# Kernel tuning notes

Hardware: AMD Instinct MI355X
Metric: run time of the kernel (lower is better)

The kernel has to match this reference:

```python
import jax, jax.numpy as jnp
import numpy as np

N_TOKENS = 65536
D_MODEL = 256
D_HID = 256
N_EXPERTS = 8


def setup_inputs() -> dict:
    key = jax.random.key(0)
    ks = jax.random.split(key, 6)
    x = jax.random.normal(ks[0], (N_TOKENS, D_MODEL), dtype=jnp.float32)
    # gate Linear weight [E, d] (torch Linear stores [out, in]); small init like nn.Linear default scale
    wg = jax.random.normal(ks[1], (N_EXPERTS, D_MODEL), dtype=jnp.float32) * 0.06
    W1 = jax.random.normal(ks[2], (N_EXPERTS, D_MODEL, D_HID), dtype=jnp.float32) * 0.06
    b1 = jnp.zeros((N_EXPERTS, D_HID), dtype=jnp.float32)
    W2 = jax.random.normal(ks[3], (N_EXPERTS, D_HID, D_MODEL), dtype=jnp.float32) * 0.06
    b2 = jnp.zeros((N_EXPERTS, D_MODEL), dtype=jnp.float32)
    return {"x": x, "wg": wg, "W1": W1, "b1": b1, "W2": W2, "b2": b2}


def reference(x, wg, W1, b1, W2, b2):
    # Gate: logits = x @ wg.T ; softmax over experts ; top-1 gate value + assignment
    gates = jax.nn.softmax(x @ wg.T, axis=1)                  # [N, E]
    gate_val = jnp.max(gates, axis=1)                          # [N] == topk(k=1) values
    assign = jnp.argmax(gates, axis=1)                         # [N] expert id per token

    out = jnp.zeros_like(x)
    # Fixed small loop over experts (structural, not data-dim); each iter is one dense GEMM pair.
    for e in range(N_EXPERTS):
        h = jax.nn.relu(x @ W1[e] + b1[e])                     # [N, D_HID]
        y_e = h @ W2[e] + b2[e]                                # [N, D_MODEL]
        sel = (assign == e)[:, None]
        out = jnp.where(sel, y_e * gate_val[:, None], out)
    return out
```

## Files before the change

kernel.cpp:

```cpp
#include <hip/hip_runtime.h>
#include <hip/hip_bf16.h>
#include <math.h>

#define NTOK 65536
#define DMODEL 256
#define NEXP 8
#define CAP 65536
#define MAXTILES 1040
#define CSTRIDE 64

typedef __bf16 bf16_t;
typedef __bf16 bf16x8 __attribute__((ext_vector_type(8)));
typedef float f32x4 __attribute__((ext_vector_type(4)));

__device__ inline void async16(const void* g, void* l) {
  __builtin_amdgcn_global_load_lds(
      (const __attribute__((address_space(1))) unsigned int*)g,
      (__attribute__((address_space(3))) unsigned int*)l, 16, 0, 0);
}

__global__ void prep_kernel(const float* __restrict__ wg, float* __restrict__ wgT,
                            int* __restrict__ counts) {
  int t = blockIdx.x * 256 + threadIdx.x;
  if (t < NEXP * DMODEL) wgT[t] = wg[(t & 7) * 256 + (t >> 3)];
  if (t < NEXP * CSTRIDE) counts[t] = 0;
}

__global__ __launch_bounds__(256) void castT_kernel(
    const float* __restrict__ W1, const float* __restrict__ W2,
    bf16_t* __restrict__ w1t, bf16_t* __restrict__ w2t) {
  __shared__ float tile[32][33];
  const int m = blockIdx.z;
  const float* src = (m < 8) ? (W1 + (size_t)m * 65536) : (W2 + (size_t)(m - 8) * 65536);
  bf16_t* dst = (m < 8) ? (w1t + (size_t)m * 65536) : (w2t + (size_t)(m - 8) * 65536);
  const int x0 = blockIdx.x * 32, y0 = blockIdx.y * 32;
  const int tx = threadIdx.x, ty = threadIdx.y;
#pragma unroll
  for (int i = 0; i < 4; ++i)
    tile[ty + i * 8][tx] = src[(size_t)(y0 + ty + i * 8) * 256 + x0 + tx];
  __syncthreads();
#pragma unroll
  for (int i = 0; i < 4; ++i)
    dst[(size_t)(x0 + ty + i * 8) * 256 + y0 + tx] = (bf16_t)tile[tx][ty + i * 8];
}

__global__ __launch_bounds__(256) void gate_kernel(
    const float* __restrict__ x, const float* __restrict__ wgT,
    bf16_t* __restrict__ xb, float* __restrict__ gateval,
    int* __restrict__ counts, int* __restrict__ idxbuf) {
  __shared__ __align__(16) float xs[64 * 256];
  __shared__ double part[3][64][9];
  const int th = threadIdx.x;
  const int lane = th & 63;
  const int wv = th >> 6;
  const int tokbase = blockIdx.x * 64;

#pragma unroll
  for (int i = 0; i < 16; ++i) {
    int p = i * 256 + th;
    int r = p >> 6;
    int c = (p & 63) ^ (r & 31);
    async16(x + (size_t)(tokbase + r) * 256 + c * 4,
            &xs[(i * 256 + wv * 64) * 4]);
  }
  __syncthreads();

#pragma unroll
  for (int i = 0; i < 8; ++i) {
    int p = i * 256 + th;
    int r = p >> 5, cb = p & 31;
    int mk = r & 31;
    f32x4 a = *(const f32x4*)&xs[r * 256 + (((2 * cb) ^ mk) * 4)];
    f32x4 b = *(const f32x4*)&xs[r * 256 + (((2 * cb + 1) ^ mk) * 4)];
    bf16x8 bv;
    bv[0] = (bf16_t)a[0]; bv[1] = (bf16_t)a[1];
    bv[2] = (bf16_t)a[2]; bv[3] = (bf16_t)a[3];
    bv[4] = (bf16_t)b[0]; bv[5] = (bf16_t)b[1];
    bv[6] = (bf16_t)b[2]; bv[7] = (bf16_t)b[3];
    *(bf16x8*)(xb + (size_t)tokbase * 256 + (size_t)p * 8) = bv;
  }

  const float* wp = wgT + wv * 64 * 8;
  const int xm = lane & 31;
  double acc[8] = {0, 0, 0, 0, 0, 0, 0, 0};
#pragma unroll
  for (int u = 0; u < 8; ++u) {
    int c0 = 16 * wv + 2 * u;
    f32x4 a = *(const f32x4*)&xs[lane * 256 + ((c0 ^ xm) * 4)];
    f32x4 b = *(const f32x4*)&xs[lane * 256 + (((c0 + 1) ^ xm) * 4)];
    float xv[8] = {a[0], a[1], a[2], a[3], b[0], b[1], b[2], b[3]};
    float s[8] = {0.f, 0.f, 0.f, 0.f, 0.f, 0.f, 0.f, 0.f};
#pragma unroll
    for (int j = 0; j < 8; ++j) {
      f32x4 w0 = *(const f32x4*)&wp[(u * 8 + j) * 8];
      f32x4 w1 = *(const f32x4*)&wp[(u * 8 + j) * 8 + 4];
      s[0] = fmaf(xv[j], w0[0], s[0]); s[1] = fmaf(xv[j], w0[1], s[1]);
      s[2] = fmaf(xv[j], w0[2], s[2]); s[3] = fmaf(xv[j], w0[3], s[3]);
      s[4] = fmaf(xv[j], w1[0], s[4]); s[5] = fmaf(xv[j], w1[1], s[5]);
      s[6] = fmaf(xv[j], w1[2], s[6]); s[7] = fmaf(xv[j], w1[3], s[7]);
    }
#pragma unroll
    for (int e = 0; e < 8; ++e) acc[e] += (double)s[e];
  }

  if (wv > 0) {
#pragma unroll
    for (int e = 0; e < 8; ++e) part[wv - 1][lane][e] = acc[e];
  }
  __syncthreads();
  if (wv == 0) {
#pragma unroll
    for (int s2 = 0; s2 < 3; ++s2)
#pragma unroll
      for (int e = 0; e < 8; ++e) acc[e] += part[s2][lane][e];
    double m = acc[0]; int bi = 0;
#pragma unroll
    for (int e = 1; e < 8; ++e) if (acc[e] > m) { m = acc[e]; bi = e; }
    float denom = 0.f;
#pragma unroll
    for (int e = 0; e < 8; ++e) denom += __expf((float)(acc[e] - m));
    const int tok = tokbase + lane;
    gateval[tok] = 1.0f / denom;
    unsigned long long mymask = 0;
#pragma unroll
    for (int e = 0; e < NEXP; ++e) {
      unsigned long long mk = __ballot(bi == e);
      if (lane == e) mymask = mk;
    }
    int mybase = 0;
    if (lane < NEXP) mybase = atomicAdd(&counts[lane * CSTRIDE], (int)__popcll(mymask));
#pragma unroll
    for (int e = 0; e < NEXP; ++e) {
      unsigned long long mk = __ballot(bi == e);
      int b = __shfl(mybase, e, 64);
      if (bi == e) {
        int pos = b + (int)__popcll(mk & ((1ull << lane) - 1ull));
        idxbuf[e * CAP + pos] = tok;
      }
    }
  }
}

__global__ void scan_kernel(const int* __restrict__ counts, int* __restrict__ bases,
                            int* __restrict__ tl, int* __restrict__ ntiles) {
  int t = threadIdx.x;
  if (t == 0) {
    int s = 0, n = 0;
    for (int e = 0; e < NEXP; ++e) {
      bases[e] = s; s += counts[e * CSTRIDE];
      n += (counts[e * CSTRIDE] + 63) >> 6;
    }
    *ntiles = n;
  }
  if (t < NEXP) {
    int off = 0;
    for (int j = 0; j < t; ++j) off += (counts[j * CSTRIDE] + 63) >> 6;
    int n = (counts[t * CSTRIDE] + 63) >> 6;
    for (int k = 0; k < n; ++k) tl[off + k] = t | (k << 3);
  }
}

__global__ __launch_bounds__(512, 4) void moe_gemm_kernel(
    const bf16_t* __restrict__ xb, const bf16_t* __restrict__ w1t,
    const bf16_t* __restrict__ w2t, const float* __restrict__ b1,
    const float* __restrict__ b2, const float* __restrict__ gateval,
    const int* __restrict__ counts, const int* __restrict__ bases,
    const int* __restrict__ idxbuf, const int* __restrict__ tl,
    const int* __restrict__ ntiles, float* __restrict__ out) {
  if ((int)blockIdx.x >= *ntiles) return;
  const int tle = tl[blockIdx.x];
  const int e = tle & 7, tm = tle >> 3;
  const int cnt = counts[e * CSTRIDE];
  (void)bases;
  __shared__ __align__(16) bf16_t ts[64 * 256];
  __shared__ int sidx[64];
  __shared__ float sgv[64];
  const int th = threadIdx.x;
  const int lane = th & 63, wv = th >> 6;
  const int lr = lane & 15, lq = lane >> 4;
  if (th < 64) {
    int r = tm * 64 + th;
    int t = idxbuf[e * CAP + (r < cnt ? r : cnt - 1)];
    sidx[th] = t;
    sgv[th] = gateval[t];
  }
  __syncthreads();
#pragma unroll
  for (int i = 0; i < 4; ++i) {
    int p = i * 512 + th;
    int r = p >> 5, s = (p & 31) ^ (r & 31);
    async16(xb + (size_t)sidx[r] * 256 + s * 8, &ts[(i * 512 + wv * 64) * 8]);
  }
  __syncthreads();

  const bf16_t* w1e = w1t + (size_t)e * 65536;
  {
    f32x4 acc[4][2] = {};
#pragma unroll
    for (int kk = 0; kk < 256; kk += 64) {
#pragma unroll
      for (int kb = 0; kb < 2; ++kb) {
        const int ks = (kk >> 3) + kb * 4 + lq;
        bf16x8 af[4], bfr[2];
#pragma unroll
        for (int mi = 0; mi < 4; ++mi) {
          int r = mi * 16 + lr;
          af[mi] = *(const bf16x8*)&ts[(r * 32 + (ks ^ (r & 31))) * 8];
        }
#pragma unroll
        for (int ni = 0; ni < 2; ++ni) {
          int n = wv * 32 + ni * 16 + lr;
          bfr[ni] = *(const bf16x8*)&w1e[(size_t)n * 256 + kk + kb * 32 + lq * 8];
        }
#pragma unroll
        for (int mi = 0; mi < 4; ++mi)
#pragma unroll
          for (int ni = 0; ni < 2; ++ni)
            acc[mi][ni] = __builtin_amdgcn_mfma_f32_16x16x32_bf16(af[mi], bfr[ni], acc[mi][ni], 0, 0, 0);
      }
    }
    float b1v[2];
#pragma unroll
    for (int ni = 0; ni < 2; ++ni) b1v[ni] = b1[e * 256 + wv * 32 + ni * 16 + lr];
    __syncthreads();
#pragma unroll
    for (int mi = 0; mi < 4; ++mi)
#pragma unroll
      for (int ni = 0; ni < 2; ++ni)
#pragma unroll
        for (int rr = 0; rr < 4; ++rr) {
          int m = mi * 16 + lq * 4 + rr;
          int n = wv * 32 + ni * 16 + lr;
          float v = acc[mi][ni][rr] + b1v[ni];
          v = v > 0.f ? v : 0.f;
          ts[(m * 32 + ((n >> 3) ^ (m & 31))) * 8 + (n & 7)] = (bf16_t)v;
        }
  }
  __syncthreads();

  const bf16_t* w2e = w2t + (size_t)e * 65536;
  {
    f32x4 acc[4][2] = {};
#pragma unroll
    for (int kk = 0; kk < 256; kk += 64) {
#pragma unroll
      for (int kb = 0; kb < 2; ++kb) {
        const int ks = (kk >> 3) + kb * 4 + lq;
        bf16x8 af[4], bfr[2];
#pragma unroll
        for (int mi = 0; mi < 4; ++mi) {
          int r = mi * 16 + lr;
          af[mi] = *(const bf16x8*)&ts[(r * 32 + (ks ^ (r & 31))) * 8];
        }
#pragma unroll
        for (int ni = 0; ni < 2; ++ni) {
          int n = wv * 32 + ni * 16 + lr;
          bfr[ni] = *(const bf16x8*)&w2e[(size_t)n * 256 + kk + kb * 32 + lq * 8];
        }
#pragma unroll
        for (int mi = 0; mi < 4; ++mi)
#pragma unroll
          for (int ni = 0; ni < 2; ++ni)
            acc[mi][ni] = __builtin_amdgcn_mfma_f32_16x16x32_bf16(af[mi], bfr[ni], acc[mi][ni], 0, 0, 0);
      }
    }
    float b2v[2];
#pragma unroll
    for (int ni = 0; ni < 2; ++ni) b2v[ni] = b2[e * 256 + wv * 32 + ni * 16 + lr];
#pragma unroll
    for (int mi = 0; mi < 4; ++mi)
#pragma unroll
      for (int rr = 0; rr < 4; ++rr) {
        int m = mi * 16 + lq * 4 + rr;
        int row = tm * 64 + m;
        if (row < cnt) {
          int tok = sidx[m];
          float g = sgv[m];
#pragma unroll
          for (int ni = 0; ni < 2; ++ni) {
            int n = wv * 32 + ni * 16 + lr;
            out[(size_t)tok * 256 + n] = (acc[mi][ni][rr] + b2v[ni]) * g;
          }
        }
      }
  }
}

extern "C" void kernel_launch(void* const* d_in, const int* in_sizes, int n_in,
                              void* d_out, int out_size, void* d_ws, size_t ws_size,
                              hipStream_t stream) {
  (void)in_sizes; (void)n_in; (void)out_size; (void)ws_size;
  const float* x  = (const float*)d_in[0];
  const float* wg = (const float*)d_in[1];
  const float* W1 = (const float*)d_in[2];
  const float* b1 = (const float*)d_in[3];
  const float* W2 = (const float*)d_in[4];
  const float* b2 = (const float*)d_in[5];
  float* out = (float*)d_out;

  char* ws = (char*)d_ws;
  size_t off = 0;
  auto alloc = [&](size_t bytes) {
    void* p = ws + off;
    off += (bytes + 255) & ~(size_t)255;
    return p;
  };
  bf16_t* xb     = (bf16_t*)alloc((size_t)NTOK * DMODEL * 2);
  bf16_t* w1t    = (bf16_t*)alloc((size_t)NEXP * 256 * 256 * 2);
  bf16_t* w2t    = (bf16_t*)alloc((size_t)NEXP * 256 * 256 * 2);
  int*    idxbuf = (int*)alloc((size_t)NEXP * CAP * 4);
  float*  gv     = (float*)alloc((size_t)NTOK * 4);
  float*  wgT    = (float*)alloc((size_t)NEXP * DMODEL * 4);
  int*    tilel  = (int*)alloc((size_t)MAXTILES * 4);
  int*    counts = (int*)alloc((size_t)NEXP * CSTRIDE * 4);
  int*    bases  = (int*)alloc(64);
  int*    ntiles = (int*)alloc(64);

  hipLaunchKernelGGL(prep_kernel, dim3(8), dim3(256), 0, stream, wg, wgT, counts);
  hipLaunchKernelGGL(castT_kernel, dim3(8, 8, 16), dim3(32, 8), 0, stream, W1, W2, w1t, w2t);
  hipLaunchKernelGGL(gate_kernel, dim3(NTOK / 64), dim3(256), 0, stream,
                     x, wgT, xb, gv, counts, idxbuf);
  hipLaunchKernelGGL(scan_kernel, dim3(1), dim3(64), 0, stream, counts, bases, tilel, ntiles);
  hipLaunchKernelGGL(moe_gemm_kernel, dim3(MAXTILES), dim3(512), 0, stream,
                     xb, w1t, w2t, b1, b2, gv, counts, bases, idxbuf, tilel, ntiles, out);
}
```

Measured before the change: 200.0 us.

## Fuse all MoE stages into one cooperative persistent kernel with grid syncs

Replaces the five separate launches (prep, weight cast/transpose, gate, scan, grouped GEMM) with a single cooperative kernel of 256 persistent blocks, separated by grid.sync barriers. Routing no longer uses global atomics: each block computes per-expert counts, the counts are shared through a small global table, and every block builds a deterministic prefix scan to place its tokens into a compact index buffer. The GEMM tiles are then distributed round-robin across the persistent blocks. The aim is to remove launch overhead and inter-kernel gaps. In exchange it adds two grid-wide barriers and uses fewer, larger blocks (256 blocks of 512 threads with about 100KB of LDS each), which may lower occupancy during the GEMM phase.

```diff
diff --git a/kernel.cpp b/kernel.cpp
--- a/kernel.cpp
+++ b/kernel.cpp
@@ -1,13 +1,15 @@
 #include <hip/hip_runtime.h>
+#include <hip/hip_cooperative_groups.h>
 #include <hip/hip_bf16.h>
 #include <math.h>
 
+namespace cg = cooperative_groups;
+
 #define NTOK 65536
-#define DMODEL 256
 #define NEXP 8
-#define CAP 65536
-#define MAXTILES 1040
-#define CSTRIDE 64
+#define NBLK 256
+#define TPB 512
+#define TOKPB 256
 
 typedef __bf16 bf16_t;
 typedef __bf16 bf16x8 __attribute__((ext_vector_type(8)));
@@ -19,270 +21,337 @@
       (__attribute__((address_space(3))) unsigned int*)l, 16, 0, 0);
 }
 
-__global__ void prep_kernel(const float* __restrict__ wg, float* __restrict__ wgT,
-                            int* __restrict__ counts) {
-  int t = blockIdx.x * 256 + threadIdx.x;
-  if (t < NEXP * DMODEL) wgT[t] = wg[(t & 7) * 256 + (t >> 3)];
-  if (t < NEXP * CSTRIDE) counts[t] = 0;
-}
-
-__global__ __launch_bounds__(256) void castT_kernel(
-    const float* __restrict__ W1, const float* __restrict__ W2,
-    bf16_t* __restrict__ w1t, bf16_t* __restrict__ w2t) {
-  __shared__ float tile[32][33];
-  const int m = blockIdx.z;
-  const float* src = (m < 8) ? (W1 + (size_t)m * 65536) : (W2 + (size_t)(m - 8) * 65536);
-  bf16_t* dst = (m < 8) ? (w1t + (size_t)m * 65536) : (w2t + (size_t)(m - 8) * 65536);
-  const int x0 = blockIdx.x * 32, y0 = blockIdx.y * 32;
-  const int tx = threadIdx.x, ty = threadIdx.y;
-#pragma unroll
-  for (int i = 0; i < 4; ++i)
-    tile[ty + i * 8][tx] = src[(size_t)(y0 + ty + i * 8) * 256 + x0 + tx];
+#define OFF_XS     0
+#define OFF_TS     0
+#define OFF_SIDX   33024
+#define OFF_SGV    33280
+#define OFF_PART   65536
+#define OFF_GTAB   65536
+#define OFF_BIL    98304
+#define OFF_LOC    99328
+#define OFF_CNTPE  100352
+#define OFF_EXCLP  100480
+#define OFF_LB     100608
+#define OFF_SB     100648
+#define OFF_TOTL   100680
+#define OFF_TOT    100712
+#define OFF_EB     100744
+#define OFF_T      100776
+#define ARENA_SZ   100784
+
+__global__ __launch_bounds__(TPB) void mega_kernel(
+    const float* __restrict__ x, const float* __restrict__ wg,
+    const float* __restrict__ W1, const float* __restrict__ b1,
+    const float* __restrict__ W2, const float* __restrict__ b2,
+    float* __restrict__ out, bf16_t* __restrict__ xb,
+    bf16_t* __restrict__ w1t, bf16_t* __restrict__ w2t,
+    int* __restrict__ idxbuf, float* __restrict__ gv,
+    int* __restrict__ gcnt) {
+  __shared__ __align__(16) char arena[ARENA_SZ];
+  float*  xs    = (float*)(arena + OFF_XS);
+  double* part  = (double*)(arena + OFF_PART);
+  int*    bil   = (int*)(arena + OFF_BIL);
+  int*    loc   = (int*)(arena + OFF_LOC);
+  int*    cntpe = (int*)(arena + OFF_CNTPE);
+  int*    exclp = (int*)(arena + OFF_EXCLP);
+  int*    lb    = (int*)(arena + OFF_LB);
+  int*    sbx   = (int*)(arena + OFF_SB);
+  int*    totl  = (int*)(arena + OFF_TOTL);
+  int*    tot   = (int*)(arena + OFF_TOT);
+  int*    ebx   = (int*)(arena + OFF_EB);
+  int*    Tsh   = (int*)(arena + OFF_T);
+
+  const int th   = threadIdx.x;
+  const int lane = th & 63;
+  const int wv   = th >> 6;
+  const int b    = blockIdx.x;
+  cg::grid_group grid = cg::this_grid();
+
+  {
+    float* tile = (float*)(arena);
+    for (int j = b; j < 1024; j += NBLK) {
+      const int m = j >> 6;
+      const int bx = (j >> 3) & 7, by = j & 7;
+      const float* src = (m < 8) ? (W1 + (size_t)m * 65536) : (W2 + (size_t)(m - 8) * 65536);
+      bf16_t* dst = (m < 8) ? (w1t + (size_t)m * 65536) : (w2t + (size_t)(m - 8) * 65536);
+      const int x0 = bx * 32, y0 = by * 32;
+      if (th < 256) {
+        int tx = th & 31, ty = th >> 5;
+#pragma unroll
+        for (int i = 0; i < 4; ++i)
+          tile[(ty + i * 8) * 33 + tx] = src[(size_t)(y0 + ty + i * 8) * 256 + x0 + tx];
+      }
+      __syncthreads();
+      if (th < 256) {
+        int tx = th & 31, ty = th >> 5;
+#pragma unroll
+        for (int i = 0; i < 4; ++i)
+          dst[(size_t)(x0 + ty + i * 8) * 256 + y0 + tx] = (bf16_t)tile[tx * 33 + ty + i * 8];
+      }
+      __syncthreads();
+    }
+  }
+
+  const int xm = lane & 31;
+  for (int p = 0; p < 4; ++p) {
+    const int tokbase = b * TOKPB + p * 64;
+#pragma unroll
+    for (int i = 0; i < 8; ++i) {
+      int q = i * 512 + th;
+      int r = q >> 6;
+      int c = (q & 63) ^ (r & 31);
+      async16(x + (size_t)(tokbase + r) * 256 + c * 4, &xs[(i * 512 + wv * 64) * 4]);
+    }
+    __syncthreads();
+#pragma unroll
+    for (int i = 0; i < 4; ++i) {
+      int q = i * 512 + th;
+      int r = q >> 5, cb = q & 31, mk = r & 31;
+      f32x4 a = *(const f32x4*)&xs[r * 256 + (((2 * cb) ^ mk) * 4)];
+      f32x4 bb = *(const f32x4*)&xs[r * 256 + (((2 * cb + 1) ^ mk) * 4)];
+      bf16x8 bv;
+      bv[0] = (bf16_t)a[0]; bv[1] = (bf16_t)a[1];
+      bv[2] = (bf16_t)a[2]; bv[3] = (bf16_t)a[3];
+      bv[4] = (bf16_t)bb[0]; bv[5] = (bf16_t)bb[1];
+      bv[6] = (bf16_t)bb[2]; bv[7] = (bf16_t)bb[3];
+      *(bf16x8*)(xb + (size_t)tokbase * 256 + (size_t)q * 8) = bv;
+    }
+    double acc[8] = {0, 0, 0, 0, 0, 0, 0, 0};
+#pragma unroll
+    for (int g = 0; g < 4; ++g) {
+      int c0 = wv * 8 + 2 * g;
+      f32x4 a = *(const f32x4*)&xs[lane * 256 + ((c0 ^ xm) * 4)];
+      f32x4 bb = *(const f32x4*)&xs[lane * 256 + (((c0 + 1) ^ xm) * 4)];
+      float xv[8] = {a[0], a[1], a[2], a[3], bb[0], bb[1], bb[2], bb[3]};
+#pragma unroll
+      for (int e = 0; e < 8; ++e) {
+        const float* wge = wg + e * 256 + wv * 32 + g * 8;
+        float s = 0.f;
+#pragma unroll
+        for (int j2 = 0; j2 < 8; ++j2) s = fmaf(xv[j2], wge[j2], s);
+        acc[e] += (double)s;
+      }
+    }
+    if (wv > 0) {
+#pragma unroll
+      for (int e = 0; e < 8; ++e) part[((wv - 1) * 64 + lane) * 9 + e] = acc[e];
+    }
+    __syncthreads();
+    if (wv == 0) {
+#pragma unroll
+      for (int s2 = 0; s2 < 7; ++s2)
+#pragma unroll
+        for (int e = 0; e < 8; ++e) acc[e] += part[(s2 * 64 + lane) * 9 + e];
+      double m = acc[0]; int bi = 0;
+#pragma unroll
+      for (int e = 1; e < 8; ++e) if (acc[e] > m) { m = acc[e]; bi = e; }
+      float denom = 0.f;
+#pragma unroll
+      for (int e = 0; e < 8; ++e) denom += __expf((float)(acc[e] - m));
+      gv[tokbase + lane] = 1.0f / denom;
+      bil[p * 64 + lane] = bi;
+    }
+    __syncthreads();
+  }
+
+  int myrank = 0, mybi = 0;
+  if (wv < 4) {
+    mybi = bil[wv * 64 + lane];
+    unsigned long long below = (1ull << lane) - 1ull;
+#pragma unroll
+    for (int e = 0; e < 8; ++e) {
+      unsigned long long mk = __ballot(mybi == e);
+      if (lane == e) cntpe[wv * 8 + e] = (int)__popcll(mk);
+      if (mybi == e) myrank = (int)__popcll(mk & below);
+    }
+  }
   __syncthreads();
-#pragma unroll
-  for (int i = 0; i < 4; ++i)
-    dst[(size_t)(x0 + ty + i * 8) * 256 + y0 + tx] = (bf16_t)tile[tx][ty + i * 8];
-}
-
-__global__ __launch_bounds__(256) void gate_kernel(
-    const float* __restrict__ x, const float* __restrict__ wgT,
-    bf16_t* __restrict__ xb, float* __restrict__ gateval,
-    int* __restrict__ counts, int* __restrict__ idxbuf) {
-  __shared__ __align__(16) float xs[64 * 256];
-  __shared__ double part[3][64][9];
-  const int th = threadIdx.x;
-  const int lane = th & 63;
-  const int wv = th >> 6;
-  const int tokbase = blockIdx.x * 64;
-
-#pragma unroll
-  for (int i = 0; i < 16; ++i) {
-    int p = i * 256 + th;
-    int r = p >> 6;
-    int c = (p & 63) ^ (r & 31);
-    async16(x + (size_t)(tokbase + r) * 256 + c * 4,
-            &xs[(i * 256 + wv * 64) * 4]);
+  if (th < 32) {
+    int w = th >> 3, e = th & 7, s = 0;
+    for (int w2 = 0; w2 < w; ++w2) s += cntpe[w2 * 8 + e];
+    exclp[th] = s;
+  }
+  if (th < 8) {
+    int s = 0;
+#pragma unroll
+    for (int w2 = 0; w2 < 4; ++w2) s += cntpe[w2 * 8 + th];
+    totl[th] = s;
+    gcnt[b * 8 + th] = s;
   }
   __syncthreads();
-
-#pragma unroll
-  for (int i = 0; i < 8; ++i) {
-    int p = i * 256 + th;
-    int r = p >> 5, cb = p & 31;
-    int mk = r & 31;
-    f32x4 a = *(const f32x4*)&xs[r * 256 + (((2 * cb) ^ mk) * 4)];
-    f32x4 b = *(const f32x4*)&xs[r * 256 + (((2 * cb + 1) ^ mk) * 4)];
-    bf16x8 bv;
-    bv[0] = (bf16_t)a[0]; bv[1] = (bf16_t)a[1];
-    bv[2] = (bf16_t)a[2]; bv[3] = (bf16_t)a[3];
-    bv[4] = (bf16_t)b[0]; bv[5] = (bf16_t)b[1];
-    bv[6] = (bf16_t)b[2]; bv[7] = (bf16_t)b[3];
-    *(bf16x8*)(xb + (size_t)tokbase * 256 + (size_t)p * 8) = bv;
-  }
-
-  const float* wp = wgT + wv * 64 * 8;
-  const int xm = lane & 31;
-  double acc[8] = {0, 0, 0, 0, 0, 0, 0, 0};
-#pragma unroll
-  for (int u = 0; u < 8; ++u) {
-    int c0 = 16 * wv + 2 * u;
-    f32x4 a = *(const f32x4*)&xs[lane * 256 + ((c0 ^ xm) * 4)];
-    f32x4 b = *(const f32x4*)&xs[lane * 256 + (((c0 + 1) ^ xm) * 4)];
-    float xv[8] = {a[0], a[1], a[2], a[3], b[0], b[1], b[2], b[3]};
-    float s[8] = {0.f, 0.f, 0.f, 0.f, 0.f, 0.f, 0.f, 0.f};
-#pragma unroll
-    for (int j = 0; j < 8; ++j) {
-      f32x4 w0 = *(const f32x4*)&wp[(u * 8 + j) * 8];
-      f32x4 w1 = *(const f32x4*)&wp[(u * 8 + j) * 8 + 4];
-      s[0] = fmaf(xv[j], w0[0], s[0]); s[1] = fmaf(xv[j], w0[1], s[1]);
-      s[2] = fmaf(xv[j], w0[2], s[2]); s[3] = fmaf(xv[j], w0[3], s[3]);
-      s[4] = fmaf(xv[j], w1[0], s[4]); s[5] = fmaf(xv[j], w1[1], s[5]);
-      s[6] = fmaf(xv[j], w1[2], s[6]); s[7] = fmaf(xv[j], w1[3], s[7]);
-    }
-#pragma unroll
-    for (int e = 0; e < 8; ++e) acc[e] += (double)s[e];
-  }
-
-  if (wv > 0) {
-#pragma unroll
-    for (int e = 0; e < 8; ++e) part[wv - 1][lane][e] = acc[e];
+  if (th == 0) {
+    lb[0] = 0;
+    for (int e = 0; e < 8; ++e) lb[e + 1] = lb[e] + totl[e];
   }
   __syncthreads();
-  if (wv == 0) {
-#pragma unroll
-    for (int s2 = 0; s2 < 3; ++s2)
-#pragma unroll
-      for (int e = 0; e < 8; ++e) acc[e] += part[s2][lane][e];
-    double m = acc[0]; int bi = 0;
-#pragma unroll
-    for (int e = 1; e < 8; ++e) if (acc[e] > m) { m = acc[e]; bi = e; }
-    float denom = 0.f;
-#pragma unroll
-    for (int e = 0; e < 8; ++e) denom += __expf((float)(acc[e] - m));
-    const int tok = tokbase + lane;
-    gateval[tok] = 1.0f / denom;
-    unsigned long long mymask = 0;
-#pragma unroll
-    for (int e = 0; e < NEXP; ++e) {
-      unsigned long long mk = __ballot(bi == e);
-      if (lane == e) mymask = mk;
-    }
-    int mybase = 0;
-    if (lane < NEXP) mybase = atomicAdd(&counts[lane * CSTRIDE], (int)__popcll(mymask));
-#pragma unroll
-    for (int e = 0; e < NEXP; ++e) {
-      unsigned long long mk = __ballot(bi == e);
-      int b = __shfl(mybase, e, 64);
-      if (bi == e) {
-        int pos = b + (int)__popcll(mk & ((1ull << lane) - 1ull));
-        idxbuf[e * CAP + pos] = tok;
-      }
-    }
-  }
-}
-
-__global__ void scan_kernel(const int* __restrict__ counts, int* __restrict__ bases,
-                            int* __restrict__ tl, int* __restrict__ ntiles) {
-  int t = threadIdx.x;
-  if (t == 0) {
-    int s = 0, n = 0;
-    for (int e = 0; e < NEXP; ++e) {
-      bases[e] = s; s += counts[e * CSTRIDE];
-      n += (counts[e * CSTRIDE] + 63) >> 6;
-    }
-    *ntiles = n;
-  }
-  if (t < NEXP) {
-    int off = 0;
-    for (int j = 0; j < t; ++j) off += (counts[j * CSTRIDE] + 63) >> 6;
-    int n = (counts[t * CSTRIDE] + 63) >> 6;
-    for (int k = 0; k < n; ++k) tl[off + k] = t | (k << 3);
-  }
-}
-
-__global__ __launch_bounds__(512, 4) void moe_gemm_kernel(
-    const bf16_t* __restrict__ xb, const bf16_t* __restrict__ w1t,
-    const bf16_t* __restrict__ w2t, const float* __restrict__ b1,
-    const float* __restrict__ b2, const float* __restrict__ gateval,
-    const int* __restrict__ counts, const int* __restrict__ bases,
-    const int* __restrict__ idxbuf, const int* __restrict__ tl,
-    const int* __restrict__ ntiles, float* __restrict__ out) {
-  if ((int)blockIdx.x >= *ntiles) return;
-  const int tle = tl[blockIdx.x];
-  const int e = tle & 7, tm = tle >> 3;
-  const int cnt = counts[e * CSTRIDE];
-  (void)bases;
-  __shared__ __align__(16) bf16_t ts[64 * 256];
-  __shared__ int sidx[64];
-  __shared__ float sgv[64];
-  const int th = threadIdx.x;
-  const int lane = th & 63, wv = th >> 6;
+  if (wv < 4) {
+    int tk = b * TOKPB + wv * 64 + lane;
+    loc[lb[mybi] + exclp[wv * 8 + mybi] + myrank] = tk | (mybi << 20);
+  }
+  __threadfence();
+  grid.sync();
+
+  {
+    int* gtab = (int*)(arena + OFF_GTAB);
+#pragma unroll
+    for (int i = 0; i < 4; ++i) gtab[i * 512 + th] = gcnt[i * 512 + th];
+    __syncthreads();
+    {
+      int e = wv, s = 0, pre = 0;
+#pragma unroll
+      for (int k = 0; k < 4; ++k) {
+        int b2 = lane * 4 + k;
+        int v = gtab[b2 * 8 + e];
+        s += v;
+        if (b2 < b) pre += v;
+      }
+#pragma unroll
+      for (int o = 1; o < 64; o <<= 1) {
+        s += __shfl_xor(s, o, 64);
+        pre += __shfl_xor(pre, o, 64);
+      }
+      if (lane == 0) { tot[e] = s; sbx[e] = pre; }
+    }
+    __syncthreads();
+    if (th == 0) {
+      int a2 = 0, Tt = 0;
+      for (int e = 0; e < 8; ++e) {
+        ebx[e] = a2; a2 += tot[e];
+        Tt += (tot[e] + 63) >> 6;
+        sbx[e] = ebx[e] + sbx[e];
+      }
+      *Tsh = Tt;
+    }
+    __syncthreads();
+    if (th < 256) {
+      int val = loc[th];
+      int bi2 = val >> 20, tk = val & 0xFFFFF;
+      idxbuf[sbx[bi2] + (th - lb[bi2])] = tk;
+    }
+  }
+  __threadfence();
+  grid.sync();
+
+  bf16_t* ts = (bf16_t*)(arena + OFF_TS);
+  int* sidx = (int*)(arena + OFF_SIDX);
+  float* sgv = (float*)(arena + OFF_SGV);
+  const int T = *Tsh;
   const int lr = lane & 15, lq = lane >> 4;
-  if (th < 64) {
-    int r = tm * 64 + th;
-    int t = idxbuf[e * CAP + (r < cnt ? r : cnt - 1)];
-    sidx[th] = t;
-    sgv[th] = gateval[t];
-  }
-  __syncthreads();
-#pragma unroll
-  for (int i = 0; i < 4; ++i) {
-    int p = i * 512 + th;
-    int r = p >> 5, s = (p & 31) ^ (r & 31);
-    async16(xb + (size_t)sidx[r] * 256 + s * 8, &ts[(i * 512 + wv * 64) * 8]);
-  }
-  __syncthreads();
-
-  const bf16_t* w1e = w1t + (size_t)e * 65536;
-  {
-    f32x4 acc[4][2] = {};
-#pragma unroll
-    for (int kk = 0; kk < 256; kk += 64) {
-#pragma unroll
-      for (int kb = 0; kb < 2; ++kb) {
-        const int ks = (kk >> 3) + kb * 4 + lq;
-        bf16x8 af[4], bfr[2];
-#pragma unroll
-        for (int mi = 0; mi < 4; ++mi) {
-          int r = mi * 16 + lr;
-          af[mi] = *(const bf16x8*)&ts[(r * 32 + (ks ^ (r & 31))) * 8];
+  for (int t = b; t < T; t += NBLK) {
+    int ex = 0, tm = 0, a2 = 0;
+#pragma unroll
+    for (int e2 = 0; e2 < 8; ++e2) {
+      int ne = (tot[e2] + 63) >> 6;
+      if (t >= a2 && t < a2 + ne) { ex = e2; tm = t - a2; }
+      a2 += ne;
+    }
+    const int ccnt = tot[ex];
+    const int base = ebx[ex];
+    if (th < 64) {
+      int r = tm * 64 + th;
+      int tk = idxbuf[base + (r < ccnt ? r : ccnt - 1)];
+      sidx[th] = tk;
+      sgv[th] = gv[tk];
+    }
+    __syncthreads();
+#pragma unroll
+    for (int i = 0; i < 4; ++i) {
+      int q = i * 512 + th;
+      int r = q >> 5, s = (q & 31) ^ (r & 31);
+      async16(xb + (size_t)sidx[r] * 256 + s * 8, &ts[(i * 512 + wv * 64) * 8]);
+    }
+    __syncthreads();
+    const bf16_t* w1e = w1t + (size_t)ex * 65536;
+    {
+      f32x4 acc[4][2] = {};
+#pragma unroll
+      for (int kk = 0; kk < 256; kk += 64) {
+#pragma unroll
+        for (int kb = 0; kb < 2; ++kb) {
+          const int ks = (kk >> 3) + kb * 4 + lq;
+          bf16x8 af[4], bfr[2];
+#pragma unroll
+          for (int mi = 0; mi < 4; ++mi) {
+            int r = mi * 16 + lr;
+            af[mi] = *(const bf16x8*)&ts[(r * 32 + (ks ^ (r & 31))) * 8];
+          }
+#pragma unroll
+          for (int ni = 0; ni < 2; ++ni) {
+            int n = wv * 32 + ni * 16 + lr;
+            bfr[ni] = *(const bf16x8*)&w1e[(size_t)n * 256 + kk + kb * 32 + lq * 8];
+          }
+#pragma unroll
+          for (int mi = 0; mi < 4; ++mi)
+#pragma unroll
+            for (int ni = 0; ni < 2; ++ni)
+              acc[mi][ni] = __builtin_amdgcn_mfma_f32_16x16x32_bf16(af[mi], bfr[ni], acc[mi][ni], 0, 0, 0);
         }
-#pragma unroll
-        for (int ni = 0; ni < 2; ++ni) {
-          int n = wv * 32 + ni * 16 + lr;
-          bfr[ni] = *(const bf16x8*)&w1e[(size_t)n * 256 + kk + kb * 32 + lq * 8];
+      }
+      float b1v[2];
+#pragma unroll
+      for (int ni = 0; ni < 2; ++ni) b1v[ni] = b1[ex * 256 + wv * 32 + ni * 16 + lr];
+      __syncthreads();
+#pragma unroll
+      for (int mi = 0; mi < 4; ++mi)
+#pragma unroll
+        for (int ni = 0; ni < 2; ++ni)
+#pragma unroll
+          for (int rr = 0; rr < 4; ++rr) {
+            int m = mi * 16 + lq * 4 + rr;
+            int n = wv * 32 + ni * 16 + lr;
+            float v = acc[mi][ni][rr] + b1v[ni];
+            v = v > 0.f ? v : 0.f;
+            ts[(m * 32 + ((n >> 3) ^ (m & 31))) * 8 + (n & 7)] = (bf16_t)v;
+          }
+    }
+    __syncthreads();
+    const bf16_t* w2e = w2t + (size_t)ex * 65536;
+    {
+      f32x4 acc[4][2] = {};
+#pragma unroll
+      for (int kk = 0; kk < 256; kk += 64) {
+#pragma unroll
+        for (int kb = 0; kb < 2; ++kb) {
+          const int ks = (kk >> 3) + kb * 4 + lq;
+          bf16x8 af[4], bfr[2];
+#pragma unroll
+          for (int mi = 0; mi < 4; ++mi) {
+            int r = mi * 16 + lr;
+            af[mi] = *(const bf16x8*)&ts[(r * 32 + (ks ^ (r & 31))) * 8];
+          }
+#pragma unroll
+          for (int ni = 0; ni < 2; ++ni) {
+            int n = wv * 32 + ni * 16 + lr;
+            bfr[ni] = *(const bf16x8*)&w2e[(size_t)n * 256 + kk + kb * 32 + lq * 8];
+          }
+#pragma unroll
+          for (int mi = 0; mi < 4; ++mi)
+#pragma unroll
+            for (int ni = 0; ni < 2; ++ni)
+              acc[mi][ni] = __builtin_amdgcn_mfma_f32_16x16x32_bf16(af[mi], bfr[ni], acc[mi][ni], 0, 0, 0);
         }
-#pragma unroll
-        for (int mi = 0; mi < 4; ++mi)
-#pragma unroll
-          for (int ni = 0; ni < 2; ++ni)
-            acc[mi][ni] = __builtin_amdgcn_mfma_f32_16x16x32_bf16(af[mi], bfr[ni], acc[mi][ni], 0, 0, 0);
-      }
-    }
-    float b1v[2];
-#pragma unroll
-    for (int ni = 0; ni < 2; ++ni) b1v[ni] = b1[e * 256 + wv * 32 + ni * 16 + lr];
-    __syncthreads();
-#pragma unroll
-    for (int mi = 0; mi < 4; ++mi)
-#pragma unroll
-      for (int ni = 0; ni < 2; ++ni)
+      }
+      float b2v[2];
+#pragma unroll
+      for (int ni = 0; ni < 2; ++ni) b2v[ni] = b2[ex * 256 + wv * 32 + ni * 16 + lr];
+#pragma unroll
+      for (int mi = 0; mi < 4; ++mi)
 #pragma unroll
         for (int rr = 0; rr < 4; ++rr) {
           int m = mi * 16 + lq * 4 + rr;
-          int n = wv * 32 + ni * 16 + lr;
-          float v = acc[mi][ni][rr] + b1v[ni];
-          v = v > 0.f ? v : 0.f;
-          ts[(m * 32 + ((n >> 3) ^ (m & 31))) * 8 + (n & 7)] = (bf16_t)v;
+          int row = tm * 64 + m;
+          if (row < ccnt) {
+            int tk = sidx[m];
+            float g = sgv[m];
+#pragma unroll
+            for (int ni = 0; ni < 2; ++ni) {
+              int n = wv * 32 + ni * 16 + lr;
+              out[(size_t)tk * 256 + n] = (acc[mi][ni][rr] + b2v[ni]) * g;
+            }
+          }
         }
-  }
-  __syncthreads();
-
-  const bf16_t* w2e = w2t + (size_t)e * 65536;
-  {
-    f32x4 acc[4][2] = {};
-#pragma unroll
-    for (int kk = 0; kk < 256; kk += 64) {
-#pragma unroll
-      for (int kb = 0; kb < 2; ++kb) {
-        const int ks = (kk >> 3) + kb * 4 + lq;
-        bf16x8 af[4], bfr[2];
-#pragma unroll
-        for (int mi = 0; mi < 4; ++mi) {
-          int r = mi * 16 + lr;
-          af[mi] = *(const bf16x8*)&ts[(r * 32 + (ks ^ (r & 31))) * 8];
-        }
-#pragma unroll
-        for (int ni = 0; ni < 2; ++ni) {
-          int n = wv * 32 + ni * 16 + lr;
-          bfr[ni] = *(const bf16x8*)&w2e[(size_t)n * 256 + kk + kb * 32 + lq * 8];
-        }
-#pragma unroll
-        for (int mi = 0; mi < 4; ++mi)
-#pragma unroll
-          for (int ni = 0; ni < 2; ++ni)
-            acc[mi][ni] = __builtin_amdgcn_mfma_f32_16x16x32_bf16(af[mi], bfr[ni], acc[mi][ni], 0, 0, 0);
-      }
-    }
-    float b2v[2];
-#pragma unroll
-    for (int ni = 0; ni < 2; ++ni) b2v[ni] = b2[e * 256 + wv * 32 + ni * 16 + lr];
-#pragma unroll
-    for (int mi = 0; mi < 4; ++mi)
-#pragma unroll
-      for (int rr = 0; rr < 4; ++rr) {
-        int m = mi * 16 + lq * 4 + rr;
-        int row = tm * 64 + m;
-        if (row < cnt) {
-          int tok = sidx[m];
-          float g = sgv[m];
-#pragma unroll
-          for (int ni = 0; ni < 2; ++ni) {
-            int n = wv * 32 + ni * 16 + lr;
-            out[(size_t)tok * 256 + n] = (acc[mi][ni][rr] + b2v[ni]) * g;
-          }
-        }
-      }
+    }
+    __syncthreads();
   }
 }
 
@@ -305,22 +374,18 @@
     off += (bytes + 255) & ~(size_t)255;
     return p;
   };
-  bf16_t* xb     = (bf16_t*)alloc((size_t)NTOK * DMODEL * 2);
+  bf16_t* xb     = (bf16_t*)alloc((size_t)NTOK * 256 * 2);
   bf16_t* w1t    = (bf16_t*)alloc((size_t)NEXP * 256 * 256 * 2);
   bf16_t* w2t    = (bf16_t*)alloc((size_t)NEXP * 256 * 256 * 2);
-  int*    idxbuf = (int*)alloc((size_t)NEXP * CAP * 4);
-  float*  gv     = (float*)alloc((size_t)NTOK * 4);
-  float*  wgT    = (float*)alloc((size_t)NEXP * DMODEL * 4);
-  int*    tilel  = (int*)alloc((size_t)MAXTILES * 4);
-  int*    counts = (int*)alloc((size_t)NEXP * CSTRIDE * 4);
-  int*    bases  = (int*)alloc(64);
-  int*    ntiles = (int*)alloc(64);
-
-  hipLaunchKernelGGL(prep_kernel, dim3(8), dim3(256), 0, stream, wg, wgT, counts);
-  hipLaunchKernelGGL(castT_kernel, dim3(8, 8, 16), dim3(32, 8), 0, stream, W1, W2, w1t, w2t);
-  hipLaunchKernelGGL(gate_kernel, dim3(NTOK / 64), dim3(256), 0, stream,
-                     x, wgT, xb, gv, counts, idxbuf);
-  hipLaunchKernelGGL(scan_kernel, dim3(1), dim3(64), 0, stream, counts, bases, tilel, ntiles);
-  hipLaunchKernelGGL(moe_gemm_kernel, dim3(MAXTILES), dim3(512), 0, stream,
-                     xb, w1t, w2t, b1, b2, gv, counts, bases, idxbuf, tilel, ntiles, out);
+  int*    idxbuf = (int*)alloc((size_t)NTOK * 4);
+  float*  gvb    = (float*)alloc((size_t)NTOK * 4);
+  int*    gcnt   = (int*)alloc((size_t)NBLK * NEXP * 4);
+
+  void* args[] = {
+    (void*)&x, (void*)&wg, (void*)&W1, (void*)&b1, (void*)&W2, (void*)&b2,
+    (void*)&out, (void*)&xb, (void*)&w1t, (void*)&w2t,
+    (void*)&idxbuf, (void*)&gvb, (void*)&gcnt
+  };
+  hipLaunchCooperativeKernel((const void*)mega_kernel, dim3(NBLK), dim3(TPB),
+                             args, 0, stream);
 }
```

Result: slower. 409.7 us (+104.8%).
